# Optimization experiments

Measured on AMD Instinct MI355X. Metric: run time of the kernel, lower is better.

The kernel has to match this reference:

```python
import jax, jax.numpy as jnp
import numpy as np

ENC_DIM = 64

def setup_inputs() -> dict:
    key = jax.random.key(0)
    ks = jax.random.split(key, 7)
    B, C, H, W = 16, 64, 128, 128
    s = 1.0 / np.sqrt(C)
    return {
        "x": jax.random.normal(ks[0], (B, C, H, W), jnp.float32),
        "wq_w": jax.random.normal(ks[1], (ENC_DIM, C), jnp.float32) * s,
        "wq_b": jax.random.normal(ks[2], (ENC_DIM,), jnp.float32) * 0.01,
        "wk_w": jax.random.normal(ks[3], (ENC_DIM, C), jnp.float32) * s,
        "wk_b": jax.random.normal(ks[4], (ENC_DIM,), jnp.float32) * 0.01,
        "wv_w": jax.random.normal(ks[5], (ENC_DIM, C), jnp.float32) * s,
        "wv_b": jax.random.normal(ks[6], (ENC_DIM,), jnp.float32) * 0.01,
    }

def _conv1x1(x, w, b):
    # 1x1 conv == per-pixel linear: [B,C,H,W] x [E,C] -> [B,E,H,W]
    return jnp.einsum('bchw,ec->behw', x, w) + b[None, :, None, None]

def reference(x, wq_w, wq_b, wk_w, wk_b, wv_w, wv_b):
    scaler = jnp.sqrt(jnp.asarray(ENC_DIM, x.dtype))
    Q = _conv1x1(x, wq_w, wq_b)  # [B,E,H,W]
    K = _conv1x1(x, wk_w, wk_b)
    V = _conv1x1(x, wv_w, wv_b)
    # scores = Q @ K^T over last two dims -> [B,E,H,H]
    scores = jnp.einsum('behw,bekw->behk', Q, K) / scaler
    temp1 = jax.nn.softmax(scores, axis=-1)          # softmax over last dim; dropout is identity (eval)
    # Q^T @ K -> [B,E,W,W], softmax over dim -2
    t2 = jnp.einsum('behw,behv->bewv', Q, K) / scaler
    temp2 = jax.nn.softmax(t2, axis=-2)
    # temp1 @ V @ temp2 -> [B,E,H,W]
    tv = jnp.einsum('behk,bekw->behw', temp1, V)
    return jnp.einsum('behw,bewv->behv', tv, temp2)
```

## Files before the change

### kernel.cpp

```cpp
#include <hip/hip_runtime.h>
#include <hip/hip_bf16.h>

typedef __attribute__((ext_vector_type(8))) short short8;
typedef __attribute__((ext_vector_type(4))) float f32x4;

#define MFMA16(a, b, c) __builtin_amdgcn_mfma_f32_16x16x32_bf16((a), (b), (c), 0, 0, 0)

__device__ __forceinline__ short f2bf(float f) {
  union { float f; unsigned u; } v; v.f = f;
  unsigned r = v.u + 0x7fffu + ((v.u >> 16) & 1u);
  return (short)(r >> 16);
}

__global__ __launch_bounds__(256) void qkv_kernel(
    const float* __restrict__ x,
    const float* __restrict__ wq, const float* __restrict__ bq,
    const float* __restrict__ wk, const float* __restrict__ bk,
    const float* __restrict__ wv, const float* __restrict__ bv,
    short* __restrict__ Q, short* __restrict__ K, short* __restrict__ V)
{
  __shared__ alignas(16) short xs[64 * 256];
  __shared__ alignas(16) short ws[3 * 64 * 64];
  __shared__ float bs[3 * 64];

  const int t    = threadIdx.x;
  const int b    = blockIdx.x >> 6;
  const int pt   = blockIdx.x & 63;
  const int pix0 = pt << 8;
  const float* xb = x + ((size_t)b << 20);

  #pragma unroll
  for (int i = 0; i < 16; ++i) {
    int f4 = i * 256 + t;
    int c  = f4 >> 6;
    int p4 = (f4 & 63) << 2;
    const float4 v = *reinterpret_cast<const float4*>(xb + c * 16384 + pix0 + p4);
    short* d = &xs[c * 256 + p4];
    d[0] = f2bf(v.x); d[1] = f2bf(v.y); d[2] = f2bf(v.z); d[3] = f2bf(v.w);
  }
  {
    #pragma unroll
    for (int i = 0; i < 16; ++i) {
      int idx = i * 256 + t;
      int e = idx >> 6, c = idx & 63;
      int d = e * 64 + (c ^ ((e & 7) << 3));
      ws[d]        = f2bf(wq[idx]);
      ws[d + 4096] = f2bf(wk[idx]);
      ws[d + 8192] = f2bf(wv[idx]);
    }
    if (t < 192) bs[t] = (t < 64) ? bq[t] : ((t < 128) ? bk[t - 64] : bv[t - 128]);
  }
  __syncthreads();

  const int lane = t & 63;
  const int wid  = t >> 6;
  const int p0   = wid << 6;
  const int l15  = lane & 15;
  const int lg   = lane >> 4;

  short8 bfrag[4][2];
  #pragma unroll
  for (int nt = 0; nt < 4; ++nt) {
    int pix = p0 + nt * 16 + l15;
    #pragma unroll
    for (int ks = 0; ks < 2; ++ks) {
      int cb = ks * 32 + (lg << 3);
      short8 f;
      #pragma unroll
      for (int j = 0; j < 8; ++j) f[j] = xs[(cb + j) * 256 + pix];
      bfrag[nt][ks] = f;
    }
  }

  #pragma unroll
  for (int m = 0; m < 3; ++m) {
    short* op = (m == 0) ? Q : ((m == 1) ? K : V);
    short8 afrag[4][2];
    #pragma unroll
    for (int mt = 0; mt < 4; ++mt) {
      int e = mt * 16 + l15;
      #pragma unroll
      for (int ks = 0; ks < 2; ++ks) {
        int cb8 = (ks * 4 + lg) ^ (e & 7);
        afrag[mt][ks] = *reinterpret_cast<const short8*>(&ws[m * 4096 + e * 64 + cb8 * 8]);
      }
    }
    #pragma unroll
    for (int mt = 0; mt < 4; ++mt) {
      #pragma unroll
      for (int nt = 0; nt < 4; ++nt) {
        f32x4 acc = {0.f, 0.f, 0.f, 0.f};
        acc = MFMA16(afrag[mt][0], bfrag[nt][0], acc);
        acc = MFMA16(afrag[mt][1], bfrag[nt][1], acc);
        int e_base = mt * 16 + (lg << 2);
        int pix = pix0 + p0 + nt * 16 + l15;
        #pragma unroll
        for (int r = 0; r < 4; ++r) {
          int e = e_base + r;
          float val = acc[r] + bs[m * 64 + e];
          op[(((size_t)b * 64 + e) << 14) + pix] = f2bf(val);
        }
      }
    }
  }
}

__global__ __launch_bounds__(512) void attn_kernel(
    const short* __restrict__ Qg, const short* __restrict__ Kg,
    const short* __restrict__ Vg, float* __restrict__ out)
{
  __shared__ alignas(16) short lds[4 * 16384];
  short* B1 = lds;
  short* B2 = lds + 16384;
  short* B3 = lds + 2 * 16384;
  short* B4 = lds + 3 * 16384;

  const int t = threadIdx.x;
  const size_t base = (size_t)blockIdx.x << 14;

  auto stage = [&](short* dst, const short* src) {
    #pragma unroll
    for (int i = 0; i < 4; ++i) {
      int eb  = i * 512 + t;
      int row = eb >> 4;
      int cb  = eb & 15;
      float4 v = *reinterpret_cast<const float4*>(src + (eb << 3));
      *reinterpret_cast<float4*>(dst + row * 128 + ((cb ^ (row & 7)) << 3)) = v;
    }
  };

  auto buildT = [&](short* dst, const short* src) {
    const int w  = t & 127;
    const int rb = (t >> 7) << 5;
    const int w7 = w & 7;
    const int wg = w >> 3;
    short v[32];
    #pragma unroll
    for (int k = 0; k < 32; ++k) {
      int r = rb + k;
      v[k] = src[r * 128 + ((wg ^ (r & 7)) << 3) + w7];
    }
    #pragma unroll
    for (int k8 = 0; k8 < 4; ++k8) {
      int hb = (rb >> 3) + k8;
      *reinterpret_cast<short8*>(&dst[w * 128 + ((hb ^ w7) << 3)]) =
          *reinterpret_cast<const short8*>(&v[k8 * 8]);
    }
  };

  const int lane = t & 63;
  const int wid  = t >> 6;
  const int m0   = wid << 4;
  const int l15  = lane & 15;
  const int lg   = lane >> 4;

  auto ldfrag = [&](const short* buf, int rowbase, int ks) -> short8 {
    int row = rowbase + l15;
    int cb  = (ks * 4 + lg) ^ (row & 7);
    return *reinterpret_cast<const short8*>(&buf[row * 128 + cb * 8]);
  };

  f32x4 acc[8];
  short8 af[4];

  auto softmax_inplace = [&]() {
    #pragma unroll
    for (int r = 0; r < 4; ++r) {
      float mx = acc[0][r];
      #pragma unroll
      for (int n = 1; n < 8; ++n) mx = fmaxf(mx, acc[n][r]);
      mx = fmaxf(mx, __shfl_xor(mx, 1));
      mx = fmaxf(mx, __shfl_xor(mx, 2));
      mx = fmaxf(mx, __shfl_xor(mx, 4));
      mx = fmaxf(mx, __shfl_xor(mx, 8));
      float s = 0.f;
      float p[8];
      #pragma unroll
      for (int n = 0; n < 8; ++n) { p[n] = __expf((acc[n][r] - mx) * 0.125f); s += p[n]; }
      s += __shfl_xor(s, 1); s += __shfl_xor(s, 2);
      s += __shfl_xor(s, 4); s += __shfl_xor(s, 8);
      float inv = 1.0f / s;
      #pragma unroll
      for (int n = 0; n < 8; ++n) acc[n][r] = p[n] * inv;
    }
  };

  auto store_strip = [&](short* dst) {
    #pragma unroll
    for (int n = 0; n < 8; ++n) {
      #pragma unroll
      for (int r = 0; r < 4; ++r) {
        int row = m0 + (lg << 2) + r;
        int col = n * 16 + l15;
        dst[row * 128 + (col ^ ((row & 7) << 3))] = f2bf(acc[n][r]);
      }
    }
  };

  stage(B1, Qg + base);
  stage(B2, Kg + base);
  __syncthreads();

  #pragma unroll
  for (int ks = 0; ks < 4; ++ks) af[ks] = ldfrag(B1, m0, ks);
  #pragma unroll
  for (int n = 0; n < 8; ++n) {
    f32x4 a = {0.f, 0.f, 0.f, 0.f};
    #pragma unroll
    for (int ks = 0; ks < 4; ++ks) a = MFMA16(af[ks], ldfrag(B2, n * 16, ks), a);
    acc[n] = a;
  }
  softmax_inplace();
  __syncthreads();

  buildT(B4, B1);
  buildT(B3, B2);
  __syncthreads();

  store_strip(B1);
  stage(B2, Vg + base);

  #pragma unroll
  for (int ks = 0; ks < 4; ++ks) af[ks] = ldfrag(B3, m0, ks);
  #pragma unroll
  for (int n = 0; n < 8; ++n) {
    f32x4 a = {0.f, 0.f, 0.f, 0.f};
    #pragma unroll
    for (int ks = 0; ks < 4; ++ks) a = MFMA16(af[ks], ldfrag(B4, n * 16, ks), a);
    acc[n] = a;
  }
  softmax_inplace();
  __syncthreads();

  store_strip(B4);
  buildT(B3, B2);
  __syncthreads();

  #pragma unroll
  for (int ks = 0; ks < 4; ++ks) af[ks] = ldfrag(B1, m0, ks);
  #pragma unroll
  for (int n = 0; n < 8; ++n) {
    f32x4 a = {0.f, 0.f, 0.f, 0.f};
    #pragma unroll
    for (int ks = 0; ks < 4; ++ks) a = MFMA16(af[ks], ldfrag(B3, n * 16, ks), a);
    acc[n] = a;
  }
  store_strip(B1);

  #pragma unroll
  for (int ks = 0; ks < 4; ++ks) af[ks] = ldfrag(B1, m0, ks);
  float* ob = out + base;
  #pragma unroll
  for (int n = 0; n < 8; ++n) {
    f32x4 a = {0.f, 0.f, 0.f, 0.f};
    #pragma unroll
    for (int ks = 0; ks < 4; ++ks) a = MFMA16(af[ks], ldfrag(B4, n * 16, ks), a);
    #pragma unroll
    for (int r = 0; r < 4; ++r) {
      int row = m0 + (lg << 2) + r;
      ob[row * 128 + n * 16 + l15] = a[r];
    }
  }
}

extern "C" void kernel_launch(void* const* d_in, const int* in_sizes, int n_in,
                              void* d_out, int out_size, void* d_ws, size_t ws_size,
                              hipStream_t stream) {
  const float* x  = (const float*)d_in[0];
  const float* wq = (const float*)d_in[1];
  const float* bq = (const float*)d_in[2];
  const float* wk = (const float*)d_in[3];
  const float* bk = (const float*)d_in[4];
  const float* wv = (const float*)d_in[5];
  const float* bv = (const float*)d_in[6];

  const size_t N = (size_t)16 * 64 * 128 * 128;
  short* Q = (short*)d_ws;
  short* K = Q + N;
  short* V = K + N;

  qkv_kernel<<<1024, 256, 0, stream>>>(x, wq, bq, wk, bk, wv, bv, Q, K, V);
  attn_kernel<<<1024, 512, 0, stream>>>(Q, K, V, (float*)d_out);
}
```

Measured before the change: 92.61 us.

## Halve attention LDS footprint by staging transposes from global and packing softmax in registers

Cuts the attention kernel's shared memory from four 32KB buffers to two. Transposed Q/K/V tiles are now built directly from global memory instead of from LDS copies, and both softmax results are held as packed bf16 pairs in registers until their buffers are free. A min-blocks hint of 4 is added to launch_bounds. The goal is to fit more workgroups per CU and hide latency, at the cost of extra strided global reads for the transposes and more register pressure.

Measured after the change: 97.36 us. 5.1% more time.

```diff
diff --git a/kernel.cpp b/kernel.cpp
--- a/kernel.cpp
+++ b/kernel.cpp
@@ -10,6 +10,9 @@
   union { float f; unsigned u; } v; v.f = f;
   unsigned r = v.u + 0x7fffu + ((v.u >> 16) & 1u);
   return (short)(r >> 16);
+}
+__device__ __forceinline__ unsigned pack2(float lo, float hi) {
+  return (unsigned)(unsigned short)f2bf(lo) | ((unsigned)(unsigned short)f2bf(hi) << 16);
 }
 
 __global__ __launch_bounds__(256) void qkv_kernel(
@@ -105,15 +108,12 @@
   }
 }
 
-__global__ __launch_bounds__(512) void attn_kernel(
+__global__ __launch_bounds__(512, 4) void attn_kernel(
     const short* __restrict__ Qg, const short* __restrict__ Kg,
     const short* __restrict__ Vg, float* __restrict__ out)
 {
-  __shared__ alignas(16) short lds[4 * 16384];
-  short* B1 = lds;
-  short* B2 = lds + 16384;
-  short* B3 = lds + 2 * 16384;
-  short* B4 = lds + 3 * 16384;
+  __shared__ alignas(16) short B1[128 * 128];
+  __shared__ alignas(16) short B2[128 * 128];
 
   const int t = threadIdx.x;
   const size_t base = (size_t)blockIdx.x << 14;
@@ -128,18 +128,13 @@
       *reinterpret_cast<float4*>(dst + row * 128 + ((cb ^ (row & 7)) << 3)) = v;
     }
   };
-
-  auto buildT = [&](short* dst, const short* src) {
+  auto stageT = [&](short* dst, const short* src) {
     const int w  = t & 127;
     const int rb = (t >> 7) << 5;
     const int w7 = w & 7;
-    const int wg = w >> 3;
     short v[32];
     #pragma unroll
-    for (int k = 0; k < 32; ++k) {
-      int r = rb + k;
-      v[k] = src[r * 128 + ((wg ^ (r & 7)) << 3) + w7];
-    }
+    for (int k = 0; k < 32; ++k) v[k] = src[(rb + k) * 128 + w];
     #pragma unroll
     for (int k8 = 0; k8 < 4; ++k8) {
       int hb = (rb >> 3) + k8;
@@ -161,9 +156,21 @@
   };
 
   f32x4 acc[8];
-  short8 af[4];
-
-  auto softmax_inplace = [&]() {
+
+  auto matmul = [&](const short* bufA, const short* bufB) {
+    short8 af[4];
+    #pragma unroll
+    for (int ks = 0; ks < 4; ++ks) af[ks] = ldfrag(bufA, m0, ks);
+    #pragma unroll
+    for (int n = 0; n < 8; ++n) {
+      f32x4 a = {0.f, 0.f, 0.f, 0.f};
+      #pragma unroll
+      for (int ks = 0; ks < 4; ++ks) a = MFMA16(af[ks], ldfrag(bufB, n * 16, ks), a);
+      acc[n] = a;
+    }
+  };
+
+  auto softmax_pack = [&](unsigned* pk) {
     #pragma unroll
     for (int r = 0; r < 4; ++r) {
       float mx = acc[0][r];
@@ -173,88 +180,80 @@
       mx = fmaxf(mx, __shfl_xor(mx, 2));
       mx = fmaxf(mx, __shfl_xor(mx, 4));
       mx = fmaxf(mx, __shfl_xor(mx, 8));
-      float s = 0.f;
-      float p[8];
+      float p[8]; float s = 0.f;
       #pragma unroll
       for (int n = 0; n < 8; ++n) { p[n] = __expf((acc[n][r] - mx) * 0.125f); s += p[n]; }
       s += __shfl_xor(s, 1); s += __shfl_xor(s, 2);
       s += __shfl_xor(s, 4); s += __shfl_xor(s, 8);
       float inv = 1.0f / s;
       #pragma unroll
-      for (int n = 0; n < 8; ++n) acc[n][r] = p[n] * inv;
-    }
-  };
-
-  auto store_strip = [&](short* dst) {
-    #pragma unroll
-    for (int n = 0; n < 8; ++n) {
-      #pragma unroll
-      for (int r = 0; r < 4; ++r) {
-        int row = m0 + (lg << 2) + r;
-        int col = n * 16 + l15;
-        dst[row * 128 + (col ^ ((row & 7) << 3))] = f2bf(acc[n][r]);
+      for (int np = 0; np < 4; ++np)
+        pk[r * 4 + np] = pack2(p[2 * np] * inv, p[2 * np + 1] * inv);
+    }
+  };
+
+  auto store_pk = [&](short* dst, const unsigned* pk) {
+    #pragma unroll
+    for (int r = 0; r < 4; ++r) {
+      int row = m0 + (lg << 2) + r;
+      int sw  = (row & 7) << 3;
+      #pragma unroll
+      for (int np = 0; np < 4; ++np) {
+        unsigned v = pk[r * 4 + np];
+        int c0 = (2 * np) * 16 + l15;
+        int c1 = c0 + 16;
+        dst[row * 128 + (c0 ^ sw)] = (short)(v & 0xffff);
+        dst[row * 128 + (c1 ^ sw)] = (short)(v >> 16);
       }
     }
   };
+
+  unsigned t1[16], t2[16];
 
   stage(B1, Qg + base);
   stage(B2, Kg + base);
   __syncthreads();
 
-  #pragma unroll
-  for (int ks = 0; ks < 4; ++ks) af[ks] = ldfrag(B1, m0, ks);
+  matmul(B1, B2);
+  softmax_pack(t1);
+  __syncthreads();
+
+  stageT(B1, Kg + base);
+  stageT(B2, Qg + base);
+  __syncthreads();
+
+  matmul(B1, B2);
+  softmax_pack(t2);
+  __syncthreads();
+
+  store_pk(B1, t1);
+  stageT(B2, Vg + base);
+  __syncthreads();
+
+  matmul(B1, B2);
+  __syncthreads();
+
   #pragma unroll
   for (int n = 0; n < 8; ++n) {
+    #pragma unroll
+    for (int r = 0; r < 4; ++r) {
+      int row = m0 + (lg << 2) + r;
+      int col = n * 16 + l15;
+      B1[row * 128 + (col ^ ((row & 7) << 3))] = f2bf(acc[n][r]);
+    }
+  }
+  store_pk(B2, t2);
+  __syncthreads();
+
+  float* ob = out + base;
+  #pragma unroll
+  for (int n = 0; n < 8; ++n) {
+    short8 af[4];
     f32x4 a = {0.f, 0.f, 0.f, 0.f};
     #pragma unroll
-    for (int ks = 0; ks < 4; ++ks) a = MFMA16(af[ks], ldfrag(B2, n * 16, ks), a);
-    acc[n] = a;
-  }
-  softmax_inplace();
-  __syncthreads();
-
-  buildT(B4, B1);
-  buildT(B3, B2);
-  __syncthreads();
-
-  store_strip(B1);
-  stage(B2, Vg + base);
-
-  #pragma unroll
-  for (int ks = 0; ks < 4; ++ks) af[ks] = ldfrag(B3, m0, ks);
-  #pragma unroll
-  for (int n = 0; n < 8; ++n) {
-    f32x4 a = {0.f, 0.f, 0.f, 0.f};
-    #pragma unroll
-    for (int ks = 0; ks < 4; ++ks) a = MFMA16(af[ks], ldfrag(B4, n * 16, ks), a);
-    acc[n] = a;
-  }
-  softmax_inplace();
-  __syncthreads();
-
-  store_strip(B4);
-  buildT(B3, B2);
-  __syncthreads();
-
-  #pragma unroll
-  for (int ks = 0; ks < 4; ++ks) af[ks] = ldfrag(B1, m0, ks);
-  #pragma unroll
-  for (int n = 0; n < 8; ++n) {
-    f32x4 a = {0.f, 0.f, 0.f, 0.f};
-    #pragma unroll
-    for (int ks = 0; ks < 4; ++ks) a = MFMA16(af[ks], ldfrag(B3, n * 16, ks), a);
-    acc[n] = a;
-  }
-  store_strip(B1);
-
-  #pragma unroll
-  for (int ks = 0; ks < 4; ++ks) af[ks] = ldfrag(B1, m0, ks);
-  float* ob = out + base;
-  #pragma unroll
-  for (int n = 0; n < 8; ++n) {
-    f32x4 a = {0.f, 0.f, 0.f, 0.f};
-    #pragma unroll
-    for (int ks = 0; ks < 4; ++ks) a = MFMA16(af[ks], ldfrag(B4, n * 16, ks), a);
+    for (int ks = 0; ks < 4; ++ks)
+      a = MFMA16(ldfrag(B1, m0, ks), ldfrag(B2, n * 16, ks), a);
+    (void)af;
     #pragma unroll
     for (int r = 0; r < 4; ++r) {
       int row = m0 + (lg << 2) + r;
```
